# Optimization experiments

Measured on AMD Instinct MI355X. Metric: run time of the kernel, lower is better.

## Reference

```python
import jax, jax.numpy as jnp
import numpy as np

EPS_CIOU = 1e-7   # keras backend epsilon used inside compute_ciou
EPS = 1e-9        # label-encoder epsilon
ALPHA = 0.5
BETA = 6.0
NUM_CLASSES = 80
TOPK = 10


def compute_ciou(b1, b2):
    """Complete IoU between xyxy boxes b1 (gt) and b2 (pred), broadcastable (...,4)."""
    x1a, y1a, x2a, y2a = b1[..., 0], b1[..., 1], b1[..., 2], b1[..., 3]
    x1b, y1b, x2b, y2b = b2[..., 0], b2[..., 1], b2[..., 2], b2[..., 3]
    w1 = x2a - x1a
    h1 = y2a - y1a + EPS_CIOU
    w2 = x2b - x1b
    h2 = y2b - y1b + EPS_CIOU
    iw = jnp.clip(jnp.minimum(x2a, x2b) - jnp.maximum(x1a, x1b), 0.0, None)
    ih = jnp.clip(jnp.minimum(y2a, y2b) - jnp.maximum(y1a, y1b), 0.0, None)
    inter = iw * ih
    union = w1 * h1 + w2 * h2 - inter
    iou = inter / (union + EPS_CIOU)
    cw = jnp.maximum(x2a, x2b) - jnp.minimum(x1a, x1b)
    ch = jnp.maximum(y2a, y2b) - jnp.minimum(y1a, y1b)
    c2 = cw * cw + ch * ch + EPS_CIOU
    rho2 = ((x1b + x2b - x1a - x2a) ** 2 + (y1b + y2b - y1a - y2a) ** 2) / 4.0
    v = (4.0 / np.pi ** 2) * (jnp.arctan(w2 / h2) - jnp.arctan(w1 / h1)) ** 2
    a = v / (v - iou + (1.0 + EPS_CIOU))
    return iou - (rho2 / c2 + v * a)


def _forward(pd_scores, pd_bboxes, anc_points, gt_labels, gt_bboxes, mask_gt):
    B, A, C = pd_scores.shape
    M = gt_bboxes.shape[1]
    f32 = pd_scores.dtype
    mask_gt_b = mask_gt.astype(bool)                      # (B, M, 1)

    # --- candidate anchors whose center falls inside each gt box ---
    lt = gt_bboxes[:, :, None, :2]                        # (B, M, 1, 2)
    rb = gt_bboxes[:, :, None, 2:]
    anc = anc_points[None, None, :, :]                    # (1, 1, A, 2)
    deltas = jnp.concatenate([anc - lt, rb - anc], -1)    # (B, M, A, 4)
    mask_in_gts = deltas.min(-1) > EPS                    # (B, M, A)
    valid = mask_in_gts & mask_gt_b                       # (B, M, A)

    # --- alignment metric: score^alpha * ciou^beta ---
    ind = gt_labels.astype(jnp.int32)                     # (B, M)
    scores_g = jnp.take_along_axis(pd_scores, jnp.maximum(ind, 0)[:, None, :], axis=-1)  # (B, A, M)
    scores_g = jnp.where(ind[:, None, :] >= 0, scores_g, 0.0)
    scores_g = jnp.transpose(scores_g, (0, 2, 1))         # (B, M, A)
    bbox_scores = jnp.where(valid, scores_g, 0.0)
    iou = compute_ciou(gt_bboxes[:, :, None, :], pd_bboxes[:, None, :, :])  # (B, M, A)
    iou = jnp.maximum(iou, 0.0)
    overlaps = jnp.where(valid, iou, 0.0)
    align_metric = bbox_scores ** ALPHA * overlaps ** BETA

    # --- top-k anchor candidates per gt box ---
    _, topk_idxs = jax.lax.top_k(align_metric, TOPK)      # (B, M, K)
    topk_mask = jnp.broadcast_to(mask_gt_b, (B, M, TOPK))
    topk_idxs = jnp.where(topk_mask, topk_idxs, 0)
    bi = jnp.arange(B)[:, None, None]
    mi = jnp.arange(M)[None, :, None]
    counts = jnp.zeros((B, M, A), f32).at[bi, mi, topk_idxs].add(1.0)
    mask_topk = jnp.where(counts > 1, 0.0, counts)        # duplicates (masked gts) -> 0
    mask_pos = mask_topk * mask_in_gts.astype(f32) * mask_gt.astype(f32)  # (B, M, A)

    # --- break ties: anchor matched to >1 gt keeps highest-IoU gt ---
    fg_mask = mask_pos.sum(axis=1)                        # (B, A)
    mask_multi = jnp.broadcast_to(fg_mask[:, None, :] > 1, (B, M, A))
    is_max = jax.nn.one_hot(jnp.argmax(overlaps, axis=1), M, dtype=f32)  # (B, A, M)
    is_max = jnp.transpose(is_max, (0, 2, 1))             # (B, M, A)
    mask_pos = jnp.where(mask_multi, is_max, mask_pos)
    fg_mask = mask_pos.sum(axis=1)
    target_gt_idx = jnp.argmax(mask_pos, axis=1)          # (B, A)

    # --- gather targets ---
    flat_idx = target_gt_idx + jnp.arange(B, dtype=target_gt_idx.dtype)[:, None] * M
    target_bboxes = gt_bboxes.reshape(-1, 4)[flat_idx]    # (B, A, 4)
    target_labels = jnp.maximum(gt_labels.reshape(-1)[flat_idx], 0.0)
    target_scores = jax.nn.one_hot(target_labels.astype(jnp.int32), C, dtype=f32)  # (B, A, C)
    target_scores = jnp.where((fg_mask > 0)[..., None], target_scores, 0.0)

    # --- normalize class targets by alignment ---
    align_metric = align_metric * mask_pos
    pos_align = align_metric.max(axis=-1, keepdims=True)              # (B, M, 1)
    pos_overlaps = (overlaps * mask_pos).max(axis=-1, keepdims=True)  # (B, M, 1)
    norm = (align_metric * pos_overlaps / (pos_align + EPS)).max(axis=-2)[..., None]  # (B, A, 1)
    target_scores = target_scores * norm

    return (jax.lax.stop_gradient(target_bboxes),
            jax.lax.stop_gradient(target_scores),
            jax.lax.stop_gradient(fg_mask > 0))


def setup_inputs() -> dict:
    key = jax.random.key(0)
    k = jax.random.split(key, 6)
    B, A, C, M = 32, 8400, 80, 64
    IMG = 640.0
    pd_scores = jax.random.uniform(k[0], (B, A, C), jnp.float32)
    pb = jax.random.uniform(k[1], (B, A, 4), jnp.float32) * IMG
    pd_bboxes = jnp.concatenate([jnp.minimum(pb[..., :2], pb[..., 2:]),
                                 jnp.maximum(pb[..., :2], pb[..., 2:])], -1)
    anc_points = jax.random.uniform(k[2], (A, 2), jnp.float32) * IMG
    ctr = jax.random.uniform(k[3], (B, M, 2), jnp.float32) * IMG
    wh = jax.random.uniform(k[4], (B, M, 2), jnp.float32) * 200.0 + 20.0
    gt_bboxes = jnp.concatenate([ctr - wh / 2, ctr + wh / 2], -1)
    gt_labels = jax.random.randint(k[5], (B, M), 0, C).astype(jnp.float32)
    mask_gt = jnp.ones((B, M, 1), jnp.bool_)
    return {"pd_scores": pd_scores, "pd_bboxes": pd_bboxes, "anc_points": anc_points,
            "gt_labels": gt_labels, "gt_bboxes": gt_bboxes, "mask_gt": mask_gt}


def reference(pd_scores, pd_bboxes, anc_points, gt_labels, gt_bboxes, mask_gt):
    return _forward(pd_scores, pd_bboxes, anc_points, gt_labels, gt_bboxes, mask_gt)
```

## Files before the change

### kernel.cpp

```cpp
#include <hip/hip_runtime.h>
#include <cstdint>
#include <cstddef>

#define EPSC 1e-7f
#define EPS9 1e-9f
#define K4PI2 0.40528473456935108577f
#define NTOPK 10
#define GX 16
#define GY 16
#define NCELL (GX * GY)

__device__ __forceinline__ bool mask_at(const unsigned char* mb, int i, int wide) {
    if (wide) return reinterpret_cast<const unsigned int*>(mb)[i] != 0u;
    return mb[i] != 0;
}

__device__ __forceinline__ unsigned long long shfl_xor_u64(unsigned long long v, int off) {
    int lo = __shfl_xor((int)(unsigned)(v & 0xFFFFFFFFull), off);
    int hi = __shfl_xor((int)(unsigned)(v >> 32), off);
    return ((unsigned long long)(unsigned)hi << 32) | (unsigned)lo;
}

__device__ __forceinline__ float ciou_clip(float x1a, float y1a, float x2a, float y2a,
                                           float w1h1, float atan1,
                                           float4 pb, float at2) {
    float w2 = pb.z - pb.x, h2 = pb.w - pb.y + EPSC;
    float iw = fmaxf(fminf(x2a, pb.z) - fmaxf(x1a, pb.x), 0.f);
    float ih = fmaxf(fminf(y2a, pb.w) - fmaxf(y1a, pb.y), 0.f);
    float inter = iw * ih;
    float uni = w1h1 + w2 * h2 - inter;
    float iou = inter / (uni + EPSC);
    float cw = fmaxf(x2a, pb.z) - fminf(x1a, pb.x);
    float ch = fmaxf(y2a, pb.w) - fminf(y1a, pb.y);
    float c2 = cw * cw + ch * ch + EPSC;
    float dx = pb.x + pb.z - x1a - x2a;
    float dy = pb.y + pb.w - y1a - y2a;
    float rho2 = (dx * dx + dy * dy) * 0.25f;
    float dat = at2 - atan1;
    float vv = K4PI2 * dat * dat;
    float aa = vv / (vv - iou + (1.f + EPSC));
    return fmaxf(iou - (rho2 / c2 + vv * aa), 0.f);
}

__global__ __launch_bounds__(1024) void k_prep(
    const unsigned char* __restrict__ mask, int nmask, int* __restrict__ mode,
    const float* __restrict__ anc, int A,
    int* __restrict__ cell_start, int* __restrict__ binned, float* __restrict__ gp)
{
    __shared__ int h[NCELL];
    __shared__ int cs[NCELL + 1];
    __shared__ int cur[NCELL];
    __shared__ float rmnx[16], rmny[16], rmxx[16], rmxy[16];
    __shared__ float s_gp[4];
    __shared__ int bad;

    int tid = threadIdx.x;
    int lane = tid & 63, wid = tid >> 6;
    const float2* an2 = reinterpret_cast<const float2*>(anc);

    if (tid == 0) bad = 0;
    if (tid < NCELL) h[tid] = 0;
    __syncthreads();

    const unsigned int* mw = reinterpret_cast<const unsigned int*>(mask);
    int nw = nmask >> 2;
    for (int i = tid; i < nw; i += 1024) {
        unsigned int v = mw[i];
        if (v != 0u && v != 1u && v != 0x3f800000u) atomicOr(&bad, 1);
    }

    float mnx = 3e38f, mny = 3e38f, mxx = -3e38f, mxy = -3e38f;
    for (int i = tid; i < A; i += 1024) {
        float2 p = an2[i];
        mnx = fminf(mnx, p.x); mny = fminf(mny, p.y);
        mxx = fmaxf(mxx, p.x); mxy = fmaxf(mxy, p.y);
    }
#pragma unroll
    for (int off = 32; off; off >>= 1) {
        mnx = fminf(mnx, __shfl_xor(mnx, off));
        mny = fminf(mny, __shfl_xor(mny, off));
        mxx = fmaxf(mxx, __shfl_xor(mxx, off));
        mxy = fmaxf(mxy, __shfl_xor(mxy, off));
    }
    if (lane == 0) { rmnx[wid] = mnx; rmny[wid] = mny; rmxx[wid] = mxx; rmxy[wid] = mxy; }
    __syncthreads();
    if (tid == 0) {
        mode[0] = bad ? 0 : 1;
        float a = 3e38f, b2 = 3e38f, c = -3e38f, d = -3e38f;
        for (int i = 0; i < 16; ++i) {
            a = fminf(a, rmnx[i]); b2 = fminf(b2, rmny[i]);
            c = fmaxf(c, rmxx[i]); d = fmaxf(d, rmxy[i]);
        }
        float rx = fmaxf(c - a, 1e-6f), ry = fmaxf(d - b2, 1e-6f);
        s_gp[0] = a; s_gp[1] = b2;
        s_gp[2] = (float)GX / rx; s_gp[3] = (float)GY / ry;
        gp[0] = s_gp[0]; gp[1] = s_gp[1]; gp[2] = s_gp[2]; gp[3] = s_gp[3];
    }
    __syncthreads();
    float ox = s_gp[0], oy = s_gp[1], ivx = s_gp[2], ivy = s_gp[3];

    for (int i = tid; i < A; i += 1024) {
        float2 p = an2[i];
        int cx = min(GX - 1, max(0, (int)floorf((p.x - ox) * ivx)));
        int cy = min(GY - 1, max(0, (int)floorf((p.y - oy) * ivy)));
        atomicAdd(&h[cy * GX + cx], 1);
    }
    __syncthreads();
    if (wid == 0) {
        int base = 0;
        for (int ch = 0; ch < NCELL / 64; ++ch) {
            int v = h[ch * 64 + lane];
            int inc = v;
            for (int off = 1; off < 64; off <<= 1) {
                int u = __shfl_up(inc, off);
                if (lane >= off) inc += u;
            }
            cs[ch * 64 + lane] = base + inc - v;
            base += __shfl(inc, 63);
        }
        if (lane == 0) cs[NCELL] = base;
    }
    __syncthreads();
    if (tid <= NCELL) cell_start[tid] = cs[tid];
    if (tid < NCELL) cur[tid] = cs[tid];
    __syncthreads();
    for (int i = tid; i < A; i += 1024) {
        float2 p = an2[i];
        int cx = min(GX - 1, max(0, (int)floorf((p.x - ox) * ivx)));
        int cy = min(GY - 1, max(0, (int)floorf((p.y - oy) * ivy)));
        int slot = atomicAdd(&cur[cy * GX + cx], 1);
        binned[slot] = i;
    }
}

__global__ __launch_bounds__(256) void k_sel(
    const float* __restrict__ pd_scores, const float* __restrict__ pd_bboxes,
    const float* __restrict__ anc, const float* __restrict__ gt_labels,
    const float* __restrict__ gt_bboxes, const unsigned char* __restrict__ mask_gt,
    const int* __restrict__ mode, const int* __restrict__ cell_start,
    const int* __restrict__ binned, const float* __restrict__ gp,
    int* __restrict__ count, int* __restrict__ win_idx, float* __restrict__ win_al,
    int* __restrict__ win_fl,
    int A, int C, int M, int B)
{
    __shared__ unsigned long long keys40[4 * NTOPK];
    __shared__ int s_pc[4];

    int bid = blockIdx.x;
    int b = bid % B, m = bid / B;
    int row = b * M + m;
    if (!mask_at(mask_gt, row, mode[0])) return;
    int tid = threadIdx.x;
    int lane = tid & 63, wid = tid >> 6;

    float4 g = reinterpret_cast<const float4*>(gt_bboxes)[row];
    float x1a = g.x, y1a = g.y, x2a = g.z, y2a = g.w;
    float w1 = x2a - x1a, h1 = y2a - y1a + EPSC;
    float w1h1 = w1 * h1;
    float atan1 = atanf(w1 / h1);
    int lbl = (int)gt_labels[row];

    float ox = gp[0], oy = gp[1], ivx = gp[2], ivy = gp[3];
    int cx0 = min(GX - 1, max(0, (int)floorf((x1a - ox) * ivx)));
    int cx1 = min(GX - 1, max(0, (int)floorf((x2a - ox) * ivx)));
    int cy0 = min(GY - 1, max(0, (int)floorf((y1a - oy) * ivy)));
    int cy1 = min(GY - 1, max(0, (int)floorf((y2a - oy) * ivy)));
    int nx = cx1 - cx0 + 1;
    int nbox = nx * (cy1 - cy0 + 1);

    const float2* an2 = reinterpret_cast<const float2*>(anc);
    const float4* pb4 = reinterpret_cast<const float4*>(pd_bboxes + (size_t)b * A * 4);
    const float*  ps  = pd_scores + (size_t)b * A * C;

    unsigned long long tv[NTOPK];
#pragma unroll
    for (int j = 0; j < NTOPK; ++j) tv[j] = 0;
    int pcnt = 0;

    for (int ci = wid; ci < nbox; ci += 4) {
        int cy = cy0 + ci / nx, cx = cx0 + ci % nx;
        int c = cy * GX + cx;
        int s = cell_start[c], e = cell_start[c + 1];
        for (int i = s + lane; i < e; i += 64) {
            int a = binned[i];
            float2 ap = an2[a];
            bool in = (ap.x - x1a > EPS9) & (ap.y - y1a > EPS9) &
                      (x2a - ap.x > EPS9) & (y2a - ap.y > EPS9);
            if (in) {
                float4 pb = pb4[a];
                float w2 = pb.z - pb.x, h2 = pb.w - pb.y + EPSC;
                float at2 = atanf(w2 / h2);
                float ovl = ciou_clip(x1a, y1a, x2a, y2a, w1h1, atan1, pb, at2);
                float sc = (lbl >= 0) ? ps[(size_t)a * C + lbl] : 0.f;
                float o2 = ovl * ovl;
                float val = sqrtf(sc) * (o2 * o2 * o2);
                pcnt += (val > 0.f) ? 1 : 0;
                unsigned long long kk =
                    ((unsigned long long)__float_as_uint(val) << 32) | (unsigned)(~(unsigned)a);
                if (kk > tv[NTOPK - 1]) {
                    tv[NTOPK - 1] = kk;
#pragma unroll
                    for (int j = NTOPK - 1; j > 0; --j)
                        if (tv[j] > tv[j - 1]) {
                            unsigned long long t = tv[j]; tv[j] = tv[j - 1]; tv[j - 1] = t;
                        }
                }
            }
        }
    }

#pragma unroll
    for (int off = 32; off; off >>= 1) pcnt += __shfl_xor(pcnt, off);
    if (lane == 0) s_pc[wid] = pcnt;
#pragma unroll
    for (int k = 0; k < NTOPK; ++k) {
        unsigned long long head = tv[0];
        unsigned long long best = head;
#pragma unroll
        for (int off = 32; off; off >>= 1) {
            unsigned long long o = shfl_xor_u64(best, off);
            if (o > best) best = o;
        }
        if (lane == 0) keys40[wid * NTOPK + k] = best;
        if (head == best && head != 0ull) {
#pragma unroll
            for (int j = 0; j < NTOPK - 1; ++j) tv[j] = tv[j + 1];
            tv[NTOPK - 1] = 0;
        }
    }
    __syncthreads();

    if (wid != 0) return;
    int p = s_pc[0] + s_pc[1] + s_pc[2] + s_pc[3];
    int rp = p < NTOPK ? p : NTOPK;
    unsigned long long key = (lane < 4 * NTOPK) ? keys40[lane] : 0;
    size_t bA = (size_t)b * A;
    int base_o = row * NTOPK;

    for (int k = 0; k < rp; ++k) {
        unsigned long long best = key;
#pragma unroll
        for (int off = 32; off; off >>= 1) {
            unsigned long long o = shfl_xor_u64(best, off);
            if (o > best) best = o;
        }
        if (key == best && best != 0ull) {
            int a = (int)(~(unsigned)(best & 0xFFFFFFFFull));
            int o = base_o + k;
            win_idx[o] = a;
            win_al[o]  = __uint_as_float((unsigned)(best >> 32));
            win_fl[o]  = 1;
            atomicAdd(&count[bA + a], 1);
            key = 0;
        }
    }

    if (rp < NTOPK) {
        int iters = (A + 63 - lane) / 64;
        int zp = 0;
        for (int k = rp; k < NTOPK; ++k) {
            unsigned zprop = 0xFFFFFFFFu;
            while (zp < iters) {
                int a = lane + zp * 64;
                float2 ap = an2[a];
                bool in = (ap.x - x1a > EPS9) & (ap.y - y1a > EPS9) &
                          (x2a - ap.x > EPS9) & (y2a - ap.y > EPS9);
                if (!in) { zprop = (unsigned)a; break; }
                ++zp;
            }
            unsigned cprop = (key != 0ull && key < (1ull << 32)) ? ~(unsigned)key : 0xFFFFFFFFu;
            unsigned prop = zprop < cprop ? zprop : cprop;
            unsigned bm_ = prop;
#pragma unroll
            for (int off = 32; off; off >>= 1) {
                unsigned o = (unsigned)__shfl_xor((int)bm_, off);
                if (o < bm_) bm_ = o;
            }
            if (bm_ != 0xFFFFFFFFu) {
                if (cprop == bm_ && cprop < zprop) {
                    int o = base_o + k;
                    win_idx[o] = (int)bm_; win_al[o] = 0.f; win_fl[o] = 1;
                    atomicAdd(&count[bA + bm_], 1);
                    key = 0;
                } else if (zprop == bm_ && zprop < cprop) {
                    ++zp;
                }
            }
        }
    }
}

__global__ void k_resolve(
    const float* __restrict__ pd_scores, const float* __restrict__ pd_bboxes,
    const float* __restrict__ anc, const float* __restrict__ gt_labels,
    const float* __restrict__ gt_bboxes, const unsigned char* __restrict__ mask_gt,
    const int* __restrict__ mode,
    const int* __restrict__ count, const int* __restrict__ win_idx,
    const float* __restrict__ win_al, const int* __restrict__ win_fl,
    int* __restrict__ claim_m, float* __restrict__ claim_al,
    float* __restrict__ pos_al, float* __restrict__ pos_ov,
    int A, int C, int M, int total)
{
    int t = blockIdx.x * 256 + threadIdx.x;
    if (t >= total) return;
    int bm = t / NTOPK;
    int b = bm / M, m = bm % M;
    if (!win_fl[t]) return;
    int a = win_idx[t];
    size_t ba = (size_t)b * A + a;
    int cnt = count[ba];
    float al, ov; int mm_out;
    if (cnt == 1) {
        mm_out = m; al = win_al[t];
        float4 gg = reinterpret_cast<const float4*>(gt_bboxes)[b * M + m];
        float w1 = gg.z - gg.x, h1 = gg.w - gg.y + EPSC;
        float4 pb = reinterpret_cast<const float4*>(pd_bboxes)[ba];
        float w2 = pb.z - pb.x, h2p = pb.w - pb.y + EPSC;
        ov = ciou_clip(gg.x, gg.y, gg.z, gg.w, w1 * h1, atanf(w1 / h1), pb, atanf(w2 / h2p));
    } else {
        int wide = mode[0];
        float4 pb = reinterpret_cast<const float4*>(pd_bboxes)[ba];
        float2 ap = reinterpret_cast<const float2*>(anc)[a];
        float w2 = pb.z - pb.x, h2p = pb.w - pb.y + EPSC;
        float at2 = atanf(w2 / h2p);
        float best_ov = -1.f; int best_m = 0, best_valid = 0;
        for (int mm = 0; mm < M; ++mm) {
            float4 gg = reinterpret_cast<const float4*>(gt_bboxes)[b * M + mm];
            bool in = (ap.x - gg.x > EPS9) && (ap.y - gg.y > EPS9) &&
                      (gg.z - ap.x > EPS9) && (gg.w - ap.y > EPS9);
            bool valid = in && mask_at(mask_gt, b * M + mm, wide);
            float ovv = 0.f;
            if (valid) {
                float w1 = gg.z - gg.x, h1 = gg.w - gg.y + EPSC;
                ovv = ciou_clip(gg.x, gg.y, gg.z, gg.w, w1 * h1, atanf(w1 / h1), pb, at2);
            }
            if (ovv > best_ov) { best_ov = ovv; best_m = mm; best_valid = valid ? 1 : 0; }
        }
        int lb = (int)gt_labels[b * M + best_m];
        float sc = (best_valid && lb >= 0) ? pd_scores[ba * C + lb] : 0.f;
        float o2 = best_ov * best_ov;
        mm_out = best_m; al = sqrtf(sc) * (o2 * o2 * o2); ov = best_ov;
    }
    claim_m[ba]  = mm_out;
    claim_al[ba] = al;
    atomicMax((unsigned int*)&pos_al[b * M + mm_out], __float_as_uint(al));
    atomicMax((unsigned int*)&pos_ov[b * M + mm_out], __float_as_uint(ov));
}

__global__ __launch_bounds__(256) void k_final(
    const int* __restrict__ count, const int* __restrict__ claim_m,
    const float* __restrict__ claim_al,
    const float* __restrict__ pos_al, const float* __restrict__ pos_ov,
    const float* __restrict__ gt_labels, const float* __restrict__ gt_bboxes,
    float* __restrict__ out_bb, float* __restrict__ out_ts, float* __restrict__ out_fg,
    int A, int M, int C4, int BA)
{
    __shared__ float s_nv[256];
    __shared__ int   s_lb[256];
    int base_ba = blockIdx.x * 256;
    int tid = threadIdx.x;
    int ba = base_ba + tid;
    if (ba < BA) {
        int b = ba / A;
        int cnt = count[ba];
        int m = claim_m[ba];
        float4 g = reinterpret_cast<const float4*>(gt_bboxes)[b * M + m];
        reinterpret_cast<float4*>(out_bb)[ba] = g;
        float nv = 0.f; int lb = -1;
        if (cnt > 0) {
            lb = max((int)gt_labels[b * M + m], 0);
            nv = claim_al[ba] * pos_ov[b * M + m] / (pos_al[b * M + m] + EPS9);
        }
        out_fg[ba] = (cnt > 0) ? 1.f : 0.f;
        s_nv[tid] = nv; s_lb[tid] = lb;
    } else { s_nv[tid] = 0.f; s_lb[tid] = -1; }
    __syncthreads();
    float4* ts4 = reinterpret_cast<float4*>(out_ts);
    size_t fbase = (size_t)base_ba * C4;
    for (int j = 0; j < C4; ++j) {
        int fl = j * 256 + tid;
        int la = fl / C4;
        int ch = fl - la * C4;
        int ba2 = base_ba + la;
        if (ba2 < BA) {
            float nv = s_nv[la];
            int lb = s_lb[la];
            int c0 = ch * 4;
            float4 o;
            o.x = (c0     == lb) ? nv : 0.f;
            o.y = (c0 + 1 == lb) ? nv : 0.f;
            o.z = (c0 + 2 == lb) ? nv : 0.f;
            o.w = (c0 + 3 == lb) ? nv : 0.f;
            ts4[fbase + fl] = o;
        }
    }
}

extern "C" void kernel_launch(void* const* d_in, const int* in_sizes, int n_in,
                              void* d_out, int out_size, void* d_ws, size_t ws_size,
                              hipStream_t stream) {
    const float* pd_scores = (const float*)d_in[0];
    const float* pd_bboxes = (const float*)d_in[1];
    const float* anc       = (const float*)d_in[2];
    const float* gt_labels = (const float*)d_in[3];
    const float* gt_bboxes = (const float*)d_in[4];
    const unsigned char* mask_gt = (const unsigned char*)d_in[5];

    int A  = in_sizes[2] / 2;
    int BA = in_sizes[1] / 4;
    int B  = BA / A;
    int C  = in_sizes[0] / BA;
    int M  = in_sizes[3] / B;
    int BM = B * M;

    char* w = (char*)d_ws;
    auto alloc = [&](size_t bytes) { char* p = w; w += ((bytes + 255) / 256) * 256; return p; };
    int*   mode       = (int*)  alloc(256);
    char*  zero_beg   = w;
    int*   count      = (int*)  alloc((size_t)BA * 4);
    int*   claim_m    = (int*)  alloc((size_t)BA * 4);
    float* pos_al     = (float*)alloc((size_t)BM * 4);
    float* pos_ov     = (float*)alloc((size_t)BM * 4);
    int*   win_fl     = (int*)  alloc((size_t)BM * NTOPK * 4);
    char*  zero_end   = w;
    float* claim_al   = (float*)alloc((size_t)BA * 4);
    int*   win_idx    = (int*)  alloc((size_t)BM * NTOPK * 4);
    float* win_al     = (float*)alloc((size_t)BM * NTOPK * 4);
    int*   cell_start = (int*)  alloc((size_t)(NCELL + 1) * 4);
    int*   binned     = (int*)  alloc((size_t)A * 4);
    float* gp         = (float*)alloc(256);

    float* out_bb = (float*)d_out;
    float* out_ts = out_bb + (size_t)BA * 4;
    float* out_fg = out_ts + (size_t)BA * C;

    hipMemsetAsync(zero_beg, 0, (size_t)(zero_end - zero_beg), stream);

    k_prep<<<1, 1024, 0, stream>>>(mask_gt, BM, mode, anc, A, cell_start, binned, gp);
    k_sel<<<BM, 256, 0, stream>>>(pd_scores, pd_bboxes, anc, gt_labels, gt_bboxes, mask_gt,
                                  mode, cell_start, binned, gp,
                                  count, win_idx, win_al, win_fl, A, C, M, B);
    int nclaims = BM * NTOPK;
    k_resolve<<<(nclaims + 255) / 256, 256, 0, stream>>>(
        pd_scores, pd_bboxes, anc, gt_labels, gt_bboxes, mask_gt, mode,
        count, win_idx, win_al, win_fl, claim_m, claim_al, pos_al, pos_ov, A, C, M, nclaims);
    int C4 = C / 4;
    int gBA = (BA + 255) / 256;
    k_final<<<gBA, 256, 0, stream>>>(count, claim_m, claim_al, pos_al, pos_ov,
                                     gt_labels, gt_bboxes, out_bb, out_ts, out_fg, A, M, C4, BA);
}
```

Baseline: 102.4 us.

## Flatten cell ranges across block and compact candidates into shared pool before top-k

The selection kernel now flattens each GT box's grid rows into one contiguous index space. All 256 threads process four candidates each with batched loads, and in-box keys are compacted via ballot/mbcnt into a shared-memory pool. A single wave then does the top-10 selection from the pool. Before, each wave walked whole cells and kept its own top-k. This targets load imbalance across cells and exposes more memory-level parallelism. If the pool overflows, the kernel records a flag and a new fallback kernel redoes that row, at the cost of one extra kernel launch and serialized single-wave top-k.

```diff
diff --git a/kernel.cpp b/kernel.cpp
--- a/kernel.cpp
+++ b/kernel.cpp
@@ -9,6 +9,7 @@
 #define GX 16
 #define GY 16
 #define NCELL (GX * GY)
+#define POOLCAP 2048
 
 __device__ __forceinline__ bool mask_at(const unsigned char* mb, int i, int wide) {
     if (wide) return reinterpret_cast<const unsigned int*>(mb)[i] != 0u;
@@ -19,6 +20,11 @@
     int lo = __shfl_xor((int)(unsigned)(v & 0xFFFFFFFFull), off);
     int hi = __shfl_xor((int)(unsigned)(v >> 32), off);
     return ((unsigned long long)(unsigned)hi << 32) | (unsigned)lo;
+}
+
+__device__ __forceinline__ unsigned lane_rank(unsigned long long ball) {
+    return __builtin_amdgcn_mbcnt_hi((unsigned)(ball >> 32),
+           __builtin_amdgcn_mbcnt_lo((unsigned)(ball & 0xFFFFFFFFull), 0u));
 }
 
 __device__ __forceinline__ float ciou_clip(float x1a, float y1a, float x2a, float y2a,
@@ -133,6 +139,9 @@
     }
 }
 
+#define INTEST(ap) ((ap.x - x1a > EPS9) & (ap.y - y1a > EPS9) & \
+                    (x2a - ap.x > EPS9) & (y2a - ap.y > EPS9))
+
 __global__ __launch_bounds__(256) void k_sel(
     const float* __restrict__ pd_scores, const float* __restrict__ pd_bboxes,
     const float* __restrict__ anc, const float* __restrict__ gt_labels,
@@ -140,11 +149,13 @@
     const int* __restrict__ mode, const int* __restrict__ cell_start,
     const int* __restrict__ binned, const float* __restrict__ gp,
     int* __restrict__ count, int* __restrict__ win_idx, float* __restrict__ win_al,
-    int* __restrict__ win_fl,
+    int* __restrict__ win_fl, int* __restrict__ ovf,
     int A, int C, int M, int B)
 {
-    __shared__ unsigned long long keys40[4 * NTOPK];
-    __shared__ int s_pc[4];
+    __shared__ unsigned long long pool[POOLCAP];
+    __shared__ int sP[GY + 1];
+    __shared__ int sB[GY];
+    __shared__ int s_n, s_ovf;
 
     int bid = blockIdx.x;
     int b = bid % B, m = bid / B;
@@ -165,27 +176,223 @@
     int cx1 = min(GX - 1, max(0, (int)floorf((x2a - ox) * ivx)));
     int cy0 = min(GY - 1, max(0, (int)floorf((y1a - oy) * ivy)));
     int cy1 = min(GY - 1, max(0, (int)floorf((y2a - oy) * ivy)));
-    int nx = cx1 - cx0 + 1;
-    int nbox = nx * (cy1 - cy0 + 1);
+    int ns = cy1 - cy0 + 1;
+
+    if (tid == 0) {
+        s_n = 0; s_ovf = 0;
+        int P = 0;
+        for (int s2 = 0; s2 < ns; ++s2) {
+            int cbase = (cy0 + s2) * GX;
+            int S = cell_start[cbase + cx0];
+            int E = cell_start[cbase + cx1 + 1];
+            sP[s2] = P; sB[s2] = S - P; P += E - S;
+        }
+        sP[ns] = P;
+    }
+    __syncthreads();
+    int L = sP[ns];
 
     const float2* an2 = reinterpret_cast<const float2*>(anc);
     const float4* pb4 = reinterpret_cast<const float4*>(pd_bboxes + (size_t)b * A * 4);
     const float*  ps  = pd_scores + (size_t)b * A * C;
 
+    int sptr = 0;
+    for (int f0 = tid; f0 < L; f0 += 1024) {
+        int f1 = f0 + 256, f2 = f0 + 512, f3 = f0 + 768;
+        bool o1 = f1 < L, o2 = f2 < L, o3 = f3 < L;
+        while (f0 >= sP[sptr + 1]) ++sptr;
+        int sl0 = sB[sptr] + f0;
+        int sp = sptr;
+        if (o1) { while (f1 >= sP[sp + 1]) ++sp; }
+        int sl1 = sB[sp] + f1;
+        if (o2) { while (f2 >= sP[sp + 1]) ++sp; }
+        int sl2 = sB[sp] + f2;
+        if (o3) { while (f3 >= sP[sp + 1]) ++sp; }
+        int sl3 = sB[sp] + f3;
+
+        int a0 = binned[sl0];
+        int a1 = o1 ? binned[sl1] : 0;
+        int a2 = o2 ? binned[sl2] : 0;
+        int a3 = o3 ? binned[sl3] : 0;
+        float2 ap0 = an2[a0], ap1 = an2[a1], ap2 = an2[a2], ap3 = an2[a3];
+        bool in0 = INTEST(ap0);
+        bool in1 = o1 & INTEST(ap1);
+        bool in2 = o2 & INTEST(ap2);
+        bool in3 = o3 & INTEST(ap3);
+
+        float4 pb0, pb1, pb2, pb3;
+        float sc0 = 0.f, sc1 = 0.f, sc2 = 0.f, sc3 = 0.f;
+        if (in0) { pb0 = pb4[a0]; if (lbl >= 0) sc0 = ps[(size_t)a0 * C + lbl]; }
+        if (in1) { pb1 = pb4[a1]; if (lbl >= 0) sc1 = ps[(size_t)a1 * C + lbl]; }
+        if (in2) { pb2 = pb4[a2]; if (lbl >= 0) sc2 = ps[(size_t)a2 * C + lbl]; }
+        if (in3) { pb3 = pb4[a3]; if (lbl >= 0) sc3 = ps[(size_t)a3 * C + lbl]; }
+
+#define PROC(ink, ak, pbk, sck) { \
+        unsigned long long key = 0; \
+        if (ink) { \
+            float w2 = pbk.z - pbk.x, h2 = pbk.w - pbk.y + EPSC; \
+            float at2 = atanf(w2 / h2); \
+            float ovl = ciou_clip(x1a, y1a, x2a, y2a, w1h1, atan1, pbk, at2); \
+            float o2v = ovl * ovl; \
+            float val = sqrtf(sck) * (o2v * o2v * o2v); \
+            key = ((unsigned long long)__float_as_uint(val) << 32) | (unsigned)(~(unsigned)ak); \
+        } \
+        unsigned long long ball = __ballot(ink); \
+        if (ball) { \
+            int bs = 0; \
+            if (lane == 0) bs = atomicAdd(&s_n, __popcll(ball)); \
+            bs = __shfl(bs, 0); \
+            if (ink) { \
+                int pos = bs + (int)lane_rank(ball); \
+                if (pos < POOLCAP) pool[pos] = key; else s_ovf = 1; \
+            } \
+        } }
+        PROC(in0, a0, pb0, sc0)
+        PROC(in1, a1, pb1, sc1)
+        PROC(in2, a2, pb2, sc2)
+        PROC(in3, a3, pb3, sc3)
+#undef PROC
+    }
+    __syncthreads();
+    if (s_ovf || s_n > POOLCAP) {
+        if (tid == 0) ovf[row] = 1;
+        return;
+    }
+    if (wid != 0) return;
+
+    int n = s_n;
     unsigned long long tv[NTOPK];
 #pragma unroll
     for (int j = 0; j < NTOPK; ++j) tv[j] = 0;
     int pcnt = 0;
-
-    for (int ci = wid; ci < nbox; ci += 4) {
-        int cy = cy0 + ci / nx, cx = cx0 + ci % nx;
-        int c = cy * GX + cx;
-        int s = cell_start[c], e = cell_start[c + 1];
+    for (int i = lane; i < n; i += 64) {
+        unsigned long long kk = pool[i];
+        pcnt += (kk >> 32) ? 1 : 0;
+        if (kk > tv[NTOPK - 1]) {
+            tv[NTOPK - 1] = kk;
+#pragma unroll
+            for (int j = NTOPK - 1; j > 0; --j)
+                if (tv[j] > tv[j - 1]) { unsigned long long t = tv[j]; tv[j] = tv[j - 1]; tv[j - 1] = t; }
+        }
+    }
+#pragma unroll
+    for (int off = 32; off; off >>= 1) pcnt += __shfl_xor(pcnt, off);
+    int p = pcnt;
+    int rp = p < NTOPK ? p : NTOPK;
+    size_t bA = (size_t)b * A;
+    int base_o = row * NTOPK;
+
+    for (int k = 0; k < rp; ++k) {
+        unsigned long long head = tv[0];
+        unsigned long long best = head;
+#pragma unroll
+        for (int off = 32; off; off >>= 1) {
+            unsigned long long o = shfl_xor_u64(best, off);
+            if (o > best) best = o;
+        }
+        if (head == best && head != 0ull) {
+            int a = (int)(~(unsigned)(best & 0xFFFFFFFFull));
+            int o = base_o + k;
+            win_idx[o] = a;
+            win_al[o]  = __uint_as_float((unsigned)(best >> 32));
+            win_fl[o]  = 1;
+            atomicAdd(&count[bA + a], 1);
+#pragma unroll
+            for (int j = 0; j < NTOPK - 1; ++j) tv[j] = tv[j + 1];
+            tv[NTOPK - 1] = 0;
+        }
+    }
+
+    if (rp < NTOPK) {
+        int iters = (A + 63 - lane) / 64;
+        int zp = 0;
+        for (int k = rp; k < NTOPK; ++k) {
+            unsigned zprop = 0xFFFFFFFFu;
+            while (zp < iters) {
+                int a = lane + zp * 64;
+                float2 ap = an2[a];
+                bool in = INTEST(ap);
+                if (!in) { zprop = (unsigned)a; break; }
+                ++zp;
+            }
+            unsigned cprop = 0xFFFFFFFFu;
+#pragma unroll
+            for (int j = 0; j < NTOPK; ++j) {
+                unsigned long long kk = tv[j];
+                if (kk != 0ull && kk < (1ull << 32)) {
+                    unsigned idx2 = ~(unsigned)kk;
+                    if (idx2 < cprop) cprop = idx2;
+                }
+            }
+            unsigned prop = zprop < cprop ? zprop : cprop;
+            unsigned bm_ = prop;
+#pragma unroll
+            for (int off = 32; off; off >>= 1) {
+                unsigned o = (unsigned)__shfl_xor((int)bm_, off);
+                if (o < bm_) bm_ = o;
+            }
+            if (bm_ != 0xFFFFFFFFu) {
+                if (cprop == bm_ && cprop < zprop) {
+                    int o = base_o + k;
+                    win_idx[o] = (int)bm_; win_al[o] = 0.f; win_fl[o] = 1;
+                    atomicAdd(&count[bA + bm_], 1);
+                    unsigned long long wkk = (unsigned long long)(unsigned)(~bm_);
+#pragma unroll
+                    for (int j = 0; j < NTOPK; ++j) if (tv[j] == wkk) tv[j] = 0;
+                } else if (zprop == bm_ && zprop < cprop) {
+                    ++zp;
+                }
+            }
+        }
+    }
+}
+
+__global__ __launch_bounds__(64) void k_sel_fb(
+    const float* __restrict__ pd_scores, const float* __restrict__ pd_bboxes,
+    const float* __restrict__ anc, const float* __restrict__ gt_labels,
+    const float* __restrict__ gt_bboxes, const unsigned char* __restrict__ mask_gt,
+    const int* __restrict__ mode, const int* __restrict__ cell_start,
+    const int* __restrict__ binned, const float* __restrict__ gp,
+    const int* __restrict__ ovf,
+    int* __restrict__ count, int* __restrict__ win_idx, float* __restrict__ win_al,
+    int* __restrict__ win_fl,
+    int A, int C, int M)
+{
+    int row = blockIdx.x;
+    if (!ovf[row]) return;
+    if (!mask_at(mask_gt, row, mode[0])) return;
+    int b = row / M;
+    int lane = threadIdx.x;
+
+    float4 g = reinterpret_cast<const float4*>(gt_bboxes)[row];
+    float x1a = g.x, y1a = g.y, x2a = g.z, y2a = g.w;
+    float w1 = x2a - x1a, h1 = y2a - y1a + EPSC;
+    float w1h1 = w1 * h1;
+    float atan1 = atanf(w1 / h1);
+    int lbl = (int)gt_labels[row];
+
+    float ox = gp[0], oy = gp[1], ivx = gp[2], ivy = gp[3];
+    int cx0 = min(GX - 1, max(0, (int)floorf((x1a - ox) * ivx)));
+    int cx1 = min(GX - 1, max(0, (int)floorf((x2a - ox) * ivx)));
+    int cy0 = min(GY - 1, max(0, (int)floorf((y1a - oy) * ivy)));
+    int cy1 = min(GY - 1, max(0, (int)floorf((y2a - oy) * ivy)));
+
+    const float2* an2 = reinterpret_cast<const float2*>(anc);
+    const float4* pb4 = reinterpret_cast<const float4*>(pd_bboxes + (size_t)b * A * 4);
+    const float*  ps  = pd_scores + (size_t)b * A * C;
+
+    unsigned long long tv[NTOPK];
+#pragma unroll
+    for (int j = 0; j < NTOPK; ++j) tv[j] = 0;
+    int pcnt = 0;
+
+    for (int cy = cy0; cy <= cy1; ++cy) {
+        int c0 = cy * GX + cx0;
+        int s = cell_start[c0], e = cell_start[cy * GX + cx1 + 1];
         for (int i = s + lane; i < e; i += 64) {
             int a = binned[i];
             float2 ap = an2[a];
-            bool in = (ap.x - x1a > EPS9) & (ap.y - y1a > EPS9) &
-                      (x2a - ap.x > EPS9) & (y2a - ap.y > EPS9);
+            bool in = INTEST(ap);
             if (in) {
                 float4 pb = pb4[a];
                 float w2 = pb.z - pb.x, h2 = pb.w - pb.y + EPSC;
@@ -211,9 +418,12 @@
 
 #pragma unroll
     for (int off = 32; off; off >>= 1) pcnt += __shfl_xor(pcnt, off);
-    if (lane == 0) s_pc[wid] = pcnt;
-#pragma unroll
-    for (int k = 0; k < NTOPK; ++k) {
+    int p = pcnt;
+    int rp = p < NTOPK ? p : NTOPK;
+    size_t bA = (size_t)b * A;
+    int base_o = row * NTOPK;
+
+    for (int k = 0; k < rp; ++k) {
         unsigned long long head = tv[0];
         unsigned long long best = head;
 #pragma unroll
@@ -221,37 +431,16 @@
             unsigned long long o = shfl_xor_u64(best, off);
             if (o > best) best = o;
         }
-        if (lane == 0) keys40[wid * NTOPK + k] = best;
         if (head == best && head != 0ull) {
-#pragma unroll
-            for (int j = 0; j < NTOPK - 1; ++j) tv[j] = tv[j + 1];
-            tv[NTOPK - 1] = 0;
-        }
-    }
-    __syncthreads();
-
-    if (wid != 0) return;
-    int p = s_pc[0] + s_pc[1] + s_pc[2] + s_pc[3];
-    int rp = p < NTOPK ? p : NTOPK;
-    unsigned long long key = (lane < 4 * NTOPK) ? keys40[lane] : 0;
-    size_t bA = (size_t)b * A;
-    int base_o = row * NTOPK;
-
-    for (int k = 0; k < rp; ++k) {
-        unsigned long long best = key;
-#pragma unroll
-        for (int off = 32; off; off >>= 1) {
-            unsigned long long o = shfl_xor_u64(best, off);
-            if (o > best) best = o;
-        }
-        if (key == best && best != 0ull) {
             int a = (int)(~(unsigned)(best & 0xFFFFFFFFull));
             int o = base_o + k;
             win_idx[o] = a;
             win_al[o]  = __uint_as_float((unsigned)(best >> 32));
             win_fl[o]  = 1;
             atomicAdd(&count[bA + a], 1);
-            key = 0;
+#pragma unroll
+            for (int j = 0; j < NTOPK - 1; ++j) tv[j] = tv[j + 1];
+            tv[NTOPK - 1] = 0;
         }
     }
 
@@ -263,12 +452,19 @@
             while (zp < iters) {
                 int a = lane + zp * 64;
                 float2 ap = an2[a];
-                bool in = (ap.x - x1a > EPS9) & (ap.y - y1a > EPS9) &
-                          (x2a - ap.x > EPS9) & (y2a - ap.y > EPS9);
+                bool in = INTEST(ap);
                 if (!in) { zprop = (unsigned)a; break; }
                 ++zp;
             }
-            unsigned cprop = (key != 0ull && key < (1ull << 32)) ? ~(unsigned)key : 0xFFFFFFFFu;
+            unsigned cprop = 0xFFFFFFFFu;
+#pragma unroll
+            for (int j = 0; j < NTOPK; ++j) {
+                unsigned long long kk = tv[j];
+                if (kk != 0ull && kk < (1ull << 32)) {
+                    unsigned idx2 = ~(unsigned)kk;
+                    if (idx2 < cprop) cprop = idx2;
+                }
+            }
             unsigned prop = zprop < cprop ? zprop : cprop;
             unsigned bm_ = prop;
 #pragma unroll
@@ -281,7 +477,9 @@
                     int o = base_o + k;
                     win_idx[o] = (int)bm_; win_al[o] = 0.f; win_fl[o] = 1;
                     atomicAdd(&count[bA + bm_], 1);
-                    key = 0;
+                    unsigned long long wkk = (unsigned long long)(unsigned)(~bm_);
+#pragma unroll
+                    for (int j = 0; j < NTOPK; ++j) if (tv[j] == wkk) tv[j] = 0;
                 } else if (zprop == bm_ && zprop < cprop) {
                     ++zp;
                 }
@@ -422,6 +620,7 @@
     float* pos_al     = (float*)alloc((size_t)BM * 4);
     float* pos_ov     = (float*)alloc((size_t)BM * 4);
     int*   win_fl     = (int*)  alloc((size_t)BM * NTOPK * 4);
+    int*   ovf        = (int*)  alloc((size_t)BM * 4);
     char*  zero_end   = w;
     float* claim_al   = (float*)alloc((size_t)BA * 4);
     int*   win_idx    = (int*)  alloc((size_t)BM * NTOPK * 4);
@@ -439,7 +638,10 @@
     k_prep<<<1, 1024, 0, stream>>>(mask_gt, BM, mode, anc, A, cell_start, binned, gp);
     k_sel<<<BM, 256, 0, stream>>>(pd_scores, pd_bboxes, anc, gt_labels, gt_bboxes, mask_gt,
                                   mode, cell_start, binned, gp,
-                                  count, win_idx, win_al, win_fl, A, C, M, B);
+                                  count, win_idx, win_al, win_fl, ovf, A, C, M, B);
+    k_sel_fb<<<BM, 64, 0, stream>>>(pd_scores, pd_bboxes, anc, gt_labels, gt_bboxes, mask_gt,
+                                    mode, cell_start, binned, gp, ovf,
+                                    count, win_idx, win_al, win_fl, A, C, M);
     int nclaims = BM * NTOPK;
     k_resolve<<<(nclaims + 255) / 256, 256, 0, stream>>>(
         pd_scores, pd_bboxes, anc, gt_labels, gt_bboxes, mask_gt, mode,
```

Result: faster. 97.08 us (-5.2%).
